# Kernel optimization log

Hardware: AMD Instinct MI355X
Metric: run time of the kernel (lower is better)

## Reference

```python
import jax, jax.numpy as jnp
import numpy as np

IN_FEATURES = 2048
OUT_FEATURES = 1024
WINDOW_SIZE = 64
NUM_WINDOWS = IN_FEATURES // WINDOW_SIZE  # branch_count = 1
TAU = 1.0
N_TOKENS = 4096


def setup_inputs() -> dict:
    key = jax.random.key(0)
    kx, kw, kt = jax.random.split(key, 3)
    x = jax.random.normal(kx, (N_TOKENS, IN_FEATURES), dtype=jnp.float32)
    # kaiming_uniform_(a=sqrt(5)) on [out,in] -> bound = 1/sqrt(in_features)
    bound = 1.0 / np.sqrt(IN_FEATURES)
    weights = jax.random.uniform(kw, (OUT_FEATURES, IN_FEATURES), dtype=jnp.float32,
                                 minval=-bound, maxval=bound)
    template_flat = 0.02 * jax.random.normal(kt, (OUT_FEATURES, NUM_WINDOWS * WINDOW_SIZE),
                                             dtype=jnp.float32)
    return {"x": x, "template_flat": template_flat, "weights": weights}


def reference(x, template_flat, weights):
    # output = Gate(x, Templates) * (x @ W.T), GLU-style.
    # Gate: per-window template projections, local |.|-softmax competition over
    # windows, global coactivation (softmax-weighted sum), SiLU nonlinearity.
    N, D = x.shape
    H = weights.shape[0]
    xw = x.reshape(N, NUM_WINDOWS, WINDOW_SIZE)                 # [N, W, S]
    tw = template_flat.reshape(H, NUM_WINDOWS, WINDOW_SIZE)     # [H, W, S]
    # per-(token, unit, window) template projection
    a = jnp.einsum('nws,hws->nhw', xw, tw)                      # [N, H, W]
    # local absolute-softmax competition over windows
    p = jax.nn.softmax(jnp.abs(a) / TAU, axis=-1)               # [N, H, W]
    # global coactivation: competition-weighted sum of window activations
    g = jnp.sum(p * a, axis=-1)                                 # [N, H]
    gate = jax.nn.silu(g)
    lin = x @ weights.T                                         # [N, H]
    return gate * lin
```

## Files before the change

kernel.cpp:

```cpp
#include <hip/hip_runtime.h>
#include <hip/hip_bf16.h>


typedef __attribute__((ext_vector_type(8))) short short8;
typedef __attribute__((ext_vector_type(4))) float f32x4;

#define N_TOK 4096
#define K_DIM 2048
#define H_DIM 1024
#define BM 128
#define BH 128
#define BK 64
#define LDSZ (BM * BK)

#define X_ELEMS (N_TOK * K_DIM)
#define W_ELEMS (H_DIM * K_DIM)
#define WS_NEED ((size_t)(X_ELEMS + 2 * W_ELEMS) * 2)

#define XB (X_ELEMS / 8 / 256)
#define WB (W_ELEMS / 8 / 256)

#define LOG2E 1.4426950408889634f
#define LN2   0.6931471805599453f

#if defined(__has_builtin)
#if __has_builtin(__builtin_amdgcn_exp2f)
#define EXP2RAW(x) __builtin_amdgcn_exp2f(x)
#endif
#endif
#ifndef EXP2RAW
__device__ __forceinline__ float exp2raw_asm(float x) {
    float r;
    asm("v_exp_f32 %0, %1" : "=v"(r) : "v"(x));
    return r;
}
#define EXP2RAW(x) exp2raw_asm(x)
#endif

__device__ __forceinline__ unsigned short f2bf(float f) {
    unsigned int u = __float_as_uint(f);
    u += 0x7FFFu + ((u >> 16) & 1u);
    return (unsigned short)(u >> 16);
}
__device__ __forceinline__ float bf2f(unsigned short h) {
    return __uint_as_float(((unsigned int)h) << 16);
}

__device__ __forceinline__ void cvt_split(f32x4 a, f32x4 b, short8& vh, short8& vl) {
#pragma unroll
    for (int i = 0; i < 4; ++i) {
        float f = a[i];
        unsigned short h = f2bf(f);
        vh[i] = (short)h;
        vl[i] = (short)f2bf(f - bf2f(h));
    }
#pragma unroll
    for (int i = 0; i < 4; ++i) {
        float f = b[i];
        unsigned short h = f2bf(f);
        vh[i + 4] = (short)h;
        vl[i + 4] = (short)f2bf(f - bf2f(h));
    }
}
__device__ __forceinline__ short8 cvt_hi(f32x4 a, f32x4 b) {
    short8 v;
#pragma unroll
    for (int i = 0; i < 4; ++i) { v[i] = (short)f2bf(a[i]); v[i + 4] = (short)f2bf(b[i]); }
    return v;
}

#define MFMA16(A, B, C) __builtin_amdgcn_mfma_f32_16x16x32_bf16(A, B, C, 0, 0, 0)

__global__ __launch_bounds__(256) void prepass_all(
    const float* __restrict__ X, const float* __restrict__ W,
    const float* __restrict__ T,
    unsigned short* __restrict__ XB_, unsigned short* __restrict__ WH,
    unsigned short* __restrict__ TH)
{
    int b = blockIdx.x;
    if (b < XB) {
        int i = b * 256 + threadIdx.x;
        const float* p = X + (size_t)i * 8;
        f32x4 a = *(const f32x4*)p;
        f32x4 c = *(const f32x4*)(p + 4);
        *(short8*)&XB_[(size_t)i * 8] = cvt_hi(a, c);
    } else if (b < XB + WB) {
        int i = (b - XB) * 256 + threadIdx.x;
        const float* p = W + (size_t)i * 8;
        f32x4 a = *(const f32x4*)p;
        f32x4 c = *(const f32x4*)(p + 4);
        *(short8*)&WH[(size_t)i * 8] = cvt_hi(a, c);
    } else {
        int i = (b - XB - WB) * 256 + threadIdx.x;
        const float* p = T + (size_t)i * 8;
        f32x4 a = *(const f32x4*)p;
        f32x4 c = *(const f32x4*)(p + 4);
#pragma unroll
        for (int j = 0; j < 4; ++j) { a[j] *= LOG2E; c[j] *= LOG2E; }
        *(short8*)&TH[(size_t)i * 8] = cvt_hi(a, c);
    }
}

#define GLL(gp, lp) __builtin_amdgcn_global_load_lds(                      \
        (const __attribute__((address_space(1))) void*)(gp),               \
        (__attribute__((address_space(3))) void*)(lp), 16, 0, 0)

__global__ __launch_bounds__(512) void dend_gemm(
    const unsigned short* __restrict__ XBp, const unsigned short* __restrict__ WH,
    const unsigned short* __restrict__ TH, float* __restrict__ O)
{
    __shared__ __align__(16) short lds[2][3][LDSZ];

    const int tid  = threadIdx.x;
    const int lane = tid & 63;
    const int wv   = tid >> 6;
    const int wm   = wv >> 2;
    const int wn   = wv & 3;

    const int bid     = blockIdx.x;
    const int logical = (bid & 7) * 32 + (bid >> 3);
    const int hb   = logical >> 5;
    const int nb   = logical & 31;
    const int row0 = nb * BM;
    const int col0 = hb * BH;

    const int srow8 = lane >> 3;
    const int schk  = (lane & 7) ^ srow8;
    const size_t xbase = (size_t)(row0 + wv * 16 + srow8) * K_DIM + schk * 8;
    const size_t wbase = (size_t)(col0 + wv * 16 + srow8) * K_DIM + schk * 8;
    const size_t rstep8 = (size_t)8 * K_DIM;
    const int dst0 = (wv * 16) * BK;
    const int dst1 = dst0 + 8 * BK;

#define STAGE(buf, t) do {                                                 \
        const size_t ko = (size_t)(t) * BK;                                \
        GLL(XBp + xbase + ko,          &lds[buf][0][dst0]);                \
        GLL(XBp + xbase + rstep8 + ko, &lds[buf][0][dst1]);                \
        GLL(WH + wbase + ko,           &lds[buf][1][dst0]);                \
        GLL(WH + wbase + rstep8 + ko,  &lds[buf][1][dst1]);                \
        GLL(TH + wbase + ko,           &lds[buf][2][dst0]);                \
        GLL(TH + wbase + rstep8 + ko,  &lds[buf][2][dst1]);                \
    } while (0)

    const int g = lane >> 4;
    int a_off[4][2], b_off[2][2];
#pragma unroll
    for (int mi = 0; mi < 4; ++mi) {
        int r = wm * 64 + mi * 16 + (lane & 15);
#pragma unroll
        for (int kc = 0; kc < 2; ++kc)
            a_off[mi][kc] = r * BK + ((kc * 4 + g) ^ (r & 7)) * 8;
    }
#pragma unroll
    for (int nj = 0; nj < 2; ++nj) {
        int r = wn * 32 + nj * 16 + (lane & 15);
#pragma unroll
        for (int kc = 0; kc < 2; ++kc)
            b_off[nj][kc] = r * BK + ((kc * 4 + g) ^ (r & 7)) * 8;
    }

    const f32x4 zeroc = (f32x4)0.0f;
    f32x4 lin[4][2], num[4][2], den[4][2], win[4][2];
#pragma unroll
    for (int mi = 0; mi < 4; ++mi)
#pragma unroll
        for (int nj = 0; nj < 2; ++nj) {
            lin[mi][nj] = zeroc; num[mi][nj] = zeroc; den[mi][nj] = zeroc;
        }

#define COMP_EPI(buf) do {                                                 \
        _Pragma("unroll")                                                  \
        for (int kc = 0; kc < 2; ++kc) {                                   \
            short8 bwh[2], bth[2];                                         \
            _Pragma("unroll")                                              \
            for (int nj = 0; nj < 2; ++nj) {                               \
                bwh[nj] = *(const short8*)&lds[buf][1][b_off[nj][kc]];     \
                bth[nj] = *(const short8*)&lds[buf][2][b_off[nj][kc]];     \
            }                                                              \
            __builtin_amdgcn_s_setprio(1);                                 \
            _Pragma("unroll")                                              \
            for (int mi = 0; mi < 4; ++mi) {                               \
                short8 ah = *(const short8*)&lds[buf][0][a_off[mi][kc]];   \
                _Pragma("unroll")                                          \
                for (int nj = 0; nj < 2; ++nj) {                           \
                    lin[mi][nj] = MFMA16(ah, bwh[nj], lin[mi][nj]);        \
                    win[mi][nj] = MFMA16(ah, bth[nj],                      \
                                         (kc == 0) ? zeroc : win[mi][nj]); \
                }                                                          \
            }                                                              \
            __builtin_amdgcn_s_setprio(0);                                 \
        }                                                                  \
        _Pragma("unroll")                                                  \
        for (int mi = 0; mi < 4; ++mi)                                     \
        _Pragma("unroll")                                                  \
        for (int nj = 0; nj < 2; ++nj)                                     \
        _Pragma("unroll")                                                  \
        for (int i = 0; i < 4; ++i) {                                      \
            float d = win[mi][nj][i];                                      \
            float e = EXP2RAW(fabsf(d));                                   \
            den[mi][nj][i] += e;                                           \
            num[mi][nj][i] = fmaf(e, d, num[mi][nj][i]);                   \
        }                                                                  \
    } while (0)

    STAGE(0, 0);
    __syncthreads();

#pragma unroll 1
    for (int w = 0; w < 16; ++w) {
        const int t0 = 2 * w;
        STAGE(1, t0 + 1);
        COMP_EPI(0);
        __syncthreads();
        if (t0 + 2 < 32) STAGE(0, t0 + 2);
        COMP_EPI(1);
        __syncthreads();
    }

#pragma unroll
    for (int mi = 0; mi < 4; ++mi)
#pragma unroll
        for (int nj = 0; nj < 2; ++nj)
#pragma unroll
            for (int i = 0; i < 4; ++i) {
                float gg   = (num[mi][nj][i] / den[mi][nj][i]) * LN2;
                float gate = gg / (1.0f + __expf(-gg));
                float val  = gate * lin[mi][nj][i];
                int r = row0 + wm * 64 + mi * 16 + (lane >> 4) * 4 + i;
                int c = col0 + wn * 32 + nj * 16 + (lane & 15);
                O[(size_t)r * H_DIM + c] = val;
            }
#undef STAGE
#undef COMP_EPI
}

__global__ __launch_bounds__(512) void dend_fused_v0(
    const float* __restrict__ X, const float* __restrict__ T,
    const float* __restrict__ W, float* __restrict__ O)
{
    __shared__ __align__(16) short lds[2][5][128 * 32];

    const int tid  = threadIdx.x;
    const int lane = tid & 63;
    const int wv   = tid >> 6;
    const int wm   = wv >> 2;
    const int wn   = wv & 3;

    const int bid     = blockIdx.x;
    const int logical = (bid & 7) * 32 + (bid >> 3);
    const int hb   = logical >> 5;
    const int nb   = logical & 31;
    const int row0 = nb * 128;
    const int col0 = hb * 128;

    const int srow  = tid >> 2;
    const int schn  = tid & 3;
    const int sslot = schn ^ ((srow >> 1) & 3);
    const int swoff = srow * 32 + sslot * 8;

    const float* gx = X + (size_t)(row0 + srow) * K_DIM + schn * 8;
    const float* gw = W + (size_t)(col0 + srow) * K_DIM + schn * 8;
    const float* gt = T + (size_t)(col0 + srow) * K_DIM + schn * 8;

    const int g = lane >> 4;
    int a_off[4], b_off[2];
#pragma unroll
    for (int mi = 0; mi < 4; ++mi) {
        int r = wm * 64 + mi * 16 + (lane & 15);
        a_off[mi] = r * 32 + (g ^ ((r >> 1) & 3)) * 8;
    }
#pragma unroll
    for (int nj = 0; nj < 2; ++nj) {
        int r = wn * 32 + nj * 16 + (lane & 15);
        b_off[nj] = r * 32 + (g ^ ((r >> 1) & 3)) * 8;
    }

    const f32x4 zeroc = (f32x4)0.0f;
    f32x4 lin[4][2], num[4][2], den[4][2], win[4][2];
#pragma unroll
    for (int mi = 0; mi < 4; ++mi)
#pragma unroll
        for (int nj = 0; nj < 2; ++nj) {
            lin[mi][nj] = zeroc; num[mi][nj] = zeroc; den[mi][nj] = zeroc;
        }

    f32x4 rx0, rx1, rw0, rw1, rt0, rt1;

#define LOADS(t) do {                                                   \
        const float* px = gx + (size_t)(t) * 32;                        \
        const float* pw = gw + (size_t)(t) * 32;                        \
        const float* pt = gt + (size_t)(t) * 32;                        \
        rx0 = *(const f32x4*)(px); rx1 = *(const f32x4*)(px + 4);       \
        rw0 = *(const f32x4*)(pw); rw1 = *(const f32x4*)(pw + 4);       \
        rt0 = *(const f32x4*)(pt); rt1 = *(const f32x4*)(pt + 4);       \
    } while (0)

#define WRITE(buf) do {                                                 \
        short8 vh, vl;                                                  \
        cvt_split(rx0, rx1, vh, vl);                                    \
        *(short8*)&lds[buf][0][swoff] = vh;                             \
        *(short8*)&lds[buf][1][swoff] = vl;                             \
        cvt_split(rw0, rw1, vh, vl);                                    \
        *(short8*)&lds[buf][2][swoff] = vh;                             \
        *(short8*)&lds[buf][3][swoff] = vl;                             \
        *(short8*)&lds[buf][4][swoff] = cvt_hi(rt0, rt1);               \
    } while (0)

#define COMPUTE(buf, ZW) do {                                           \
        short8 bwh[2], bwl[2], bth[2];                                  \
        _Pragma("unroll")                                               \
        for (int nj = 0; nj < 2; ++nj) {                                \
            bwh[nj] = *(const short8*)&lds[buf][2][b_off[nj]];          \
            bwl[nj] = *(const short8*)&lds[buf][3][b_off[nj]];          \
            bth[nj] = *(const short8*)&lds[buf][4][b_off[nj]];          \
        }                                                               \
        _Pragma("unroll")                                               \
        for (int mi = 0; mi < 4; ++mi) {                                \
            short8 ah = *(const short8*)&lds[buf][0][a_off[mi]];        \
            short8 al = *(const short8*)&lds[buf][1][a_off[mi]];        \
            _Pragma("unroll")                                           \
            for (int nj = 0; nj < 2; ++nj) {                            \
                lin[mi][nj] = MFMA16(ah, bwh[nj], lin[mi][nj]);         \
                lin[mi][nj] = MFMA16(al, bwh[nj], lin[mi][nj]);         \
                lin[mi][nj] = MFMA16(ah, bwl[nj], lin[mi][nj]);         \
                win[mi][nj] = MFMA16(ah, bth[nj], (ZW) ? zeroc : win[mi][nj]); \
            }                                                           \
        }                                                               \
    } while (0)

#define EPILOG() do {                                                   \
        _Pragma("unroll")                                               \
        for (int mi = 0; mi < 4; ++mi)                                  \
        _Pragma("unroll")                                               \
        for (int nj = 0; nj < 2; ++nj)                                  \
        _Pragma("unroll")                                               \
        for (int i = 0; i < 4; ++i) {                                   \
            float d = win[mi][nj][i];                                   \
            float e = __expf(fabsf(d));                                 \
            den[mi][nj][i] += e;                                        \
            num[mi][nj][i] = fmaf(e, d, num[mi][nj][i]);                \
        }                                                               \
    } while (0)

    LOADS(0);
    WRITE(0);
    __syncthreads();

#pragma unroll 1
    for (int w = 0; w < 32; ++w) {
        const int t0 = 2 * w;
        LOADS(t0 + 1);
        COMPUTE(0, true);
        __syncthreads();
        WRITE(1);
        __syncthreads();
        const bool more = (w < 31);
        if (more) LOADS(t0 + 2);
        COMPUTE(1, false);
        EPILOG();
        __syncthreads();
        if (more) WRITE(0);
        __syncthreads();
    }

#pragma unroll
    for (int mi = 0; mi < 4; ++mi)
#pragma unroll
        for (int nj = 0; nj < 2; ++nj)
#pragma unroll
            for (int i = 0; i < 4; ++i) {
                float gg   = num[mi][nj][i] / den[mi][nj][i];
                float gate = gg / (1.0f + __expf(-gg));
                float val  = gate * lin[mi][nj][i];
                int r = row0 + wm * 64 + mi * 16 + (lane >> 4) * 4 + i;
                int c = col0 + wn * 32 + nj * 16 + (lane & 15);
                O[(size_t)r * H_DIM + c] = val;
            }
#undef LOADS
#undef WRITE
#undef COMPUTE
#undef EPILOG
}

extern "C" void kernel_launch(void* const* d_in, const int* in_sizes, int n_in,
                              void* d_out, int out_size, void* d_ws, size_t ws_size,
                              hipStream_t stream) {
    const float* X = (const float*)d_in[0];
    const float* T = (const float*)d_in[1];
    const float* W = (const float*)d_in[2];
    float* O = (float*)d_out;
    (void)in_sizes; (void)n_in; (void)out_size;

    if (ws_size >= WS_NEED) {
        unsigned short* XBp = (unsigned short*)d_ws;
        unsigned short* WHp = XBp + X_ELEMS;
        unsigned short* THp = WHp + W_ELEMS;
        prepass_all<<<XB + 2 * WB, 256, 0, stream>>>(X, W, T, XBp, WHp, THp);
        dend_gemm<<<256, 512, 0, stream>>>(XBp, WHp, THp, O);
    } else {
        dend_fused_v0<<<256, 512, 0, stream>>>(X, T, W, O);
    }
}
```

Before: 64.52 us.

## Shrink GEMM tile to 128x64 with BK=32 and launch 512 blocks

Halves the output tile width (BH 128→64) and the K-step (64→32), so the grid doubles to 512 blocks and per-thread accumulators drop from 32 to 16 f32x4. The staging plan changes so half the waves load W and half load T. The swizzle and the block-index remap are updated to match. The aim is better CU occupancy and lower register and LDS pressure, paid for with less reuse of X per loaded tile, twice as many K iterations and barriers, and reloading X for twice as many column blocks.

```diff
diff --git a/kernel.cpp b/kernel.cpp
--- a/kernel.cpp
+++ b/kernel.cpp
@@ -9,16 +9,15 @@
 #define K_DIM 2048
 #define H_DIM 1024
 #define BM 128
-#define BH 128
-#define BK 64
-#define LDSZ (BM * BK)
+#define BH 64
+#define BK 32
 
 #define X_ELEMS (N_TOK * K_DIM)
 #define W_ELEMS (H_DIM * K_DIM)
 #define WS_NEED ((size_t)(X_ELEMS + 2 * W_ELEMS) * 2)
 
-#define XB (X_ELEMS / 8 / 256)
-#define WB (W_ELEMS / 8 / 256)
+#define XBLK (X_ELEMS / 8 / 256)
+#define WBLK (W_ELEMS / 8 / 256)
 
 #define LOG2E 1.4426950408889634f
 #define LN2   0.6931471805599453f
@@ -78,20 +77,20 @@
     unsigned short* __restrict__ TH)
 {
     int b = blockIdx.x;
-    if (b < XB) {
+    if (b < XBLK) {
         int i = b * 256 + threadIdx.x;
         const float* p = X + (size_t)i * 8;
         f32x4 a = *(const f32x4*)p;
         f32x4 c = *(const f32x4*)(p + 4);
         *(short8*)&XB_[(size_t)i * 8] = cvt_hi(a, c);
-    } else if (b < XB + WB) {
-        int i = (b - XB) * 256 + threadIdx.x;
+    } else if (b < XBLK + WBLK) {
+        int i = (b - XBLK) * 256 + threadIdx.x;
         const float* p = W + (size_t)i * 8;
         f32x4 a = *(const f32x4*)p;
         f32x4 c = *(const f32x4*)(p + 4);
         *(short8*)&WH[(size_t)i * 8] = cvt_hi(a, c);
     } else {
-        int i = (b - XB - WB) * 256 + threadIdx.x;
+        int i = (b - XBLK - WBLK) * 256 + threadIdx.x;
         const float* p = T + (size_t)i * 8;
         f32x4 a = *(const f32x4*)p;
         f32x4 c = *(const f32x4*)(p + 4);
@@ -109,7 +108,8 @@
     const unsigned short* __restrict__ XBp, const unsigned short* __restrict__ WH,
     const unsigned short* __restrict__ TH, float* __restrict__ O)
 {
-    __shared__ __align__(16) short lds[2][3][LDSZ];
+    __shared__ __align__(16) short ldsx[2][BM * BK];
+    __shared__ __align__(16) short ldsb[2][2][BH * BK];
 
     const int tid  = threadIdx.x;
     const int lane = tid & 63;
@@ -118,88 +118,68 @@
     const int wn   = wv & 3;
 
     const int bid     = blockIdx.x;
-    const int logical = (bid & 7) * 32 + (bid >> 3);
-    const int hb   = logical >> 5;
-    const int nb   = logical & 31;
+    const int logical = (bid & 7) * 64 + (bid >> 3);
+    const int nb   = logical >> 4;
+    const int hb   = logical & 15;
     const int row0 = nb * BM;
     const int col0 = hb * BH;
 
-    const int srow8 = lane >> 3;
-    const int schk  = (lane & 7) ^ srow8;
-    const size_t xbase = (size_t)(row0 + wv * 16 + srow8) * K_DIM + schk * 8;
-    const size_t wbase = (size_t)(col0 + wv * 16 + srow8) * K_DIM + schk * 8;
-    const size_t rstep8 = (size_t)8 * K_DIM;
-    const int dst0 = (wv * 16) * BK;
-    const int dst1 = dst0 + 8 * BK;
+    const int srow = lane >> 2;
+    const int sc   = (lane & 3) ^ ((lane >> 3) & 3);
+    const size_t xbase = (size_t)(row0 + wv * 16 + srow) * K_DIM + sc * 8;
+    const unsigned short* bsrc = (wv < 4) ? WH : TH;
+    const int barr = wv >> 2;
+    const size_t bbase = (size_t)(col0 + (wv & 3) * 16 + srow) * K_DIM + sc * 8;
+    const int dstx = (wv * 16) * BK;
+    const int dstb = ((wv & 3) * 16) * BK;
 
 #define STAGE(buf, t) do {                                                 \
         const size_t ko = (size_t)(t) * BK;                                \
-        GLL(XBp + xbase + ko,          &lds[buf][0][dst0]);                \
-        GLL(XBp + xbase + rstep8 + ko, &lds[buf][0][dst1]);                \
-        GLL(WH + wbase + ko,           &lds[buf][1][dst0]);                \
-        GLL(WH + wbase + rstep8 + ko,  &lds[buf][1][dst1]);                \
-        GLL(TH + wbase + ko,           &lds[buf][2][dst0]);                \
-        GLL(TH + wbase + rstep8 + ko,  &lds[buf][2][dst1]);                \
+        GLL(XBp + xbase + ko, &ldsx[buf][dstx]);                           \
+        GLL(bsrc + bbase + ko, &ldsb[buf][barr][dstb]);                    \
     } while (0)
 
     const int g = lane >> 4;
-    int a_off[4][2], b_off[2][2];
+    int a_off[4], b_off;
 #pragma unroll
     for (int mi = 0; mi < 4; ++mi) {
         int r = wm * 64 + mi * 16 + (lane & 15);
-#pragma unroll
-        for (int kc = 0; kc < 2; ++kc)
-            a_off[mi][kc] = r * BK + ((kc * 4 + g) ^ (r & 7)) * 8;
-    }
-#pragma unroll
-    for (int nj = 0; nj < 2; ++nj) {
-        int r = wn * 32 + nj * 16 + (lane & 15);
-#pragma unroll
-        for (int kc = 0; kc < 2; ++kc)
-            b_off[nj][kc] = r * BK + ((kc * 4 + g) ^ (r & 7)) * 8;
+        a_off[mi] = r * BK + ((g ^ ((r >> 1) & 3)) * 8);
+    }
+    {
+        int r = wn * 16 + (lane & 15);
+        b_off = r * BK + ((g ^ ((r >> 1) & 3)) * 8);
     }
 
     const f32x4 zeroc = (f32x4)0.0f;
-    f32x4 lin[4][2], num[4][2], den[4][2], win[4][2];
-#pragma unroll
-    for (int mi = 0; mi < 4; ++mi)
-#pragma unroll
-        for (int nj = 0; nj < 2; ++nj) {
-            lin[mi][nj] = zeroc; num[mi][nj] = zeroc; den[mi][nj] = zeroc;
-        }
-
-#define COMP_EPI(buf) do {                                                 \
+    f32x4 lin[4], num[4], den[4], win[4];
+#pragma unroll
+    for (int mi = 0; mi < 4; ++mi) {
+        lin[mi] = zeroc; num[mi] = zeroc; den[mi] = zeroc;
+    }
+
+#define COMPUTE(buf, ZW) do {                                              \
+        short8 bw = *(const short8*)&ldsb[buf][0][b_off];                  \
+        short8 bt = *(const short8*)&ldsb[buf][1][b_off];                  \
+        __builtin_amdgcn_s_setprio(1);                                     \
         _Pragma("unroll")                                                  \
-        for (int kc = 0; kc < 2; ++kc) {                                   \
-            short8 bwh[2], bth[2];                                         \
-            _Pragma("unroll")                                              \
-            for (int nj = 0; nj < 2; ++nj) {                               \
-                bwh[nj] = *(const short8*)&lds[buf][1][b_off[nj][kc]];     \
-                bth[nj] = *(const short8*)&lds[buf][2][b_off[nj][kc]];     \
-            }                                                              \
-            __builtin_amdgcn_s_setprio(1);                                 \
-            _Pragma("unroll")                                              \
-            for (int mi = 0; mi < 4; ++mi) {                               \
-                short8 ah = *(const short8*)&lds[buf][0][a_off[mi][kc]];   \
-                _Pragma("unroll")                                          \
-                for (int nj = 0; nj < 2; ++nj) {                           \
-                    lin[mi][nj] = MFMA16(ah, bwh[nj], lin[mi][nj]);        \
-                    win[mi][nj] = MFMA16(ah, bth[nj],                      \
-                                         (kc == 0) ? zeroc : win[mi][nj]); \
-                }                                                          \
-            }                                                              \
-            __builtin_amdgcn_s_setprio(0);                                 \
+        for (int mi = 0; mi < 4; ++mi) {                                   \
+            short8 ah = *(const short8*)&ldsx[buf][a_off[mi]];             \
+            lin[mi] = MFMA16(ah, bw, lin[mi]);                             \
+            win[mi] = MFMA16(ah, bt, (ZW) ? zeroc : win[mi]);              \
         }                                                                  \
+        __builtin_amdgcn_s_setprio(0);                                     \
+    } while (0)
+
+#define EPILOG() do {                                                      \
         _Pragma("unroll")                                                  \
         for (int mi = 0; mi < 4; ++mi)                                     \
         _Pragma("unroll")                                                  \
-        for (int nj = 0; nj < 2; ++nj)                                     \
-        _Pragma("unroll")                                                  \
         for (int i = 0; i < 4; ++i) {                                      \
-            float d = win[mi][nj][i];                                      \
+            float d = win[mi][i];                                          \
             float e = EXP2RAW(fabsf(d));                                   \
-            den[mi][nj][i] += e;                                           \
-            num[mi][nj][i] = fmaf(e, d, num[mi][nj][i]);                   \
+            den[mi][i] += e;                                               \
+            num[mi][i] = fmaf(e, d, num[mi][i]);                           \
         }                                                                  \
     } while (0)
 
@@ -207,31 +187,31 @@
     __syncthreads();
 
 #pragma unroll 1
-    for (int w = 0; w < 16; ++w) {
+    for (int w = 0; w < 32; ++w) {
         const int t0 = 2 * w;
         STAGE(1, t0 + 1);
-        COMP_EPI(0);
-        __syncthreads();
-        if (t0 + 2 < 32) STAGE(0, t0 + 2);
-        COMP_EPI(1);
+        COMPUTE(0, true);
+        __syncthreads();
+        if (t0 + 2 < 64) STAGE(0, t0 + 2);
+        COMPUTE(1, false);
+        EPILOG();
         __syncthreads();
     }
 
 #pragma unroll
     for (int mi = 0; mi < 4; ++mi)
 #pragma unroll
-        for (int nj = 0; nj < 2; ++nj)
-#pragma unroll
-            for (int i = 0; i < 4; ++i) {
-                float gg   = (num[mi][nj][i] / den[mi][nj][i]) * LN2;
-                float gate = gg / (1.0f + __expf(-gg));
-                float val  = gate * lin[mi][nj][i];
-                int r = row0 + wm * 64 + mi * 16 + (lane >> 4) * 4 + i;
-                int c = col0 + wn * 32 + nj * 16 + (lane & 15);
-                O[(size_t)r * H_DIM + c] = val;
-            }
+        for (int i = 0; i < 4; ++i) {
+            float gg   = (num[mi][i] / den[mi][i]) * LN2;
+            float gate = gg / (1.0f + __expf(-gg));
+            float val  = gate * lin[mi][i];
+            int r = row0 + wm * 64 + mi * 16 + (lane >> 4) * 4 + i;
+            int c = col0 + wn * 16 + (lane & 15);
+            O[(size_t)r * H_DIM + c] = val;
+        }
 #undef STAGE
-#undef COMP_EPI
+#undef COMPUTE
+#undef EPILOG
 }
 
 __global__ __launch_bounds__(512) void dend_fused_v0(
@@ -395,8 +375,8 @@
         unsigned short* XBp = (unsigned short*)d_ws;
         unsigned short* WHp = XBp + X_ELEMS;
         unsigned short* THp = WHp + W_ELEMS;
-        prepass_all<<<XB + 2 * WB, 256, 0, stream>>>(X, W, T, XBp, WHp, THp);
-        dend_gemm<<<256, 512, 0, stream>>>(XBp, WHp, THp, O);
+        prepass_all<<<XBLK + 2 * WBLK, 256, 0, stream>>>(X, W, T, XBp, WHp, THp);
+        dend_gemm<<<512, 512, 0, stream>>>(XBp, WHp, THp, O);
     } else {
         dend_fused_v0<<<256, 512, 0, stream>>>(X, T, W, O);
     }
```

Measured after the change: 68.41 us. 1.06x slower.
